# Kernel tuning notes

Measured on AMD Instinct MI355X. Metric: run time of the kernel, lower is better.

Reference implementation:

```python
import jax, jax.numpy as jnp
import numpy as np
from jax.scipy.special import erf

# ---- static config (mirrors module __init__) ----
G = 64          # graphs per batch
N = 64          # atoms per graph (equal-size graphs)
T = G * N       # total atoms
NUM_TYPES = 4
DEG = 32        # avg neighbors per atom
E = T * DEG
F = 128         # node feature dim
R_MAX = 6.0
R_IN = 1.0
EPS = 0.5       # fill value for distance matrix / cross-graph gamma
Q_TOT = 0.0


def setup_inputs() -> dict:
    key = jax.random.key(0)
    ks = jax.random.split(key, 12)
    batch = jnp.repeat(jnp.arange(G, dtype=jnp.int64), N)
    types = jax.random.randint(ks[0], (T,), 0, NUM_TYPES)
    node_attrs = jax.nn.one_hot(types, NUM_TYPES, dtype=jnp.float32)
    # within-graph random edges, symmetrized
    src = jax.random.randint(ks[1], (E // 2,), 0, T)
    dst = (src // N) * N + jax.random.randint(ks[2], (E // 2,), 0, N)
    edge_index = jnp.stack([jnp.concatenate([src, dst]),
                            jnp.concatenate([dst, src])]).astype(jnp.int64)
    half_len = jax.random.uniform(ks[3], (E // 2,), minval=1.0, maxval=R_MAX, dtype=jnp.float32)
    edge_length = jnp.concatenate([half_len, half_len])[:, None]
    kappa = jax.random.normal(ks[4], (T,), dtype=jnp.float32)
    node_feats = jax.random.normal(ks[5], (T, F), dtype=jnp.float32)
    ref_eta = jax.random.uniform(ks[6], (NUM_TYPES,), minval=0.5, maxval=1.5, dtype=jnp.float32)
    ref_log_sigma = jax.random.normal(ks[7], (NUM_TYPES,), dtype=jnp.float32) * 0.1
    ref_A = jax.random.uniform(ks[8], (NUM_TYPES, NUM_TYPES), minval=10.0, maxval=50.0, dtype=jnp.float32)
    ref_B = jax.random.uniform(ks[9], (NUM_TYPES, NUM_TYPES), minval=2.0, maxval=4.0, dtype=jnp.float32)
    ref_C = jax.random.uniform(ks[10], (NUM_TYPES, NUM_TYPES), minval=100.0, maxval=300.0, dtype=jnp.float32)
    ref_D = jnp.zeros((NUM_TYPES, NUM_TYPES), dtype=jnp.float32)
    ref_mu = jax.random.uniform(ks[11], (NUM_TYPES, NUM_TYPES), minval=0.8, maxval=1.2, dtype=jnp.float32)
    # symmetrize pairwise refs (type-pair parameters)
    sym = lambda m: 0.5 * (m + m.T)
    short_energy = jax.random.normal(jax.random.fold_in(key, 100), (G, 1), dtype=jnp.float32)
    atomic_short_energy = jax.random.normal(jax.random.fold_in(key, 101), (T, 1), dtype=jnp.float32)
    return dict(batch=batch, node_attrs=node_attrs, edge_index=edge_index,
                edge_length=edge_length, kappa=kappa, node_feats=node_feats,
                ref_eta=ref_eta, ref_log_sigma=ref_log_sigma,
                ref_A=sym(ref_A), ref_B=sym(ref_B), ref_C=sym(ref_C),
                ref_D=ref_D, ref_mu=sym(ref_mu),
                short_energy=short_energy, atomic_short_energy=atomic_short_energy)


def _f_cut(R):
    c1 = jnp.tanh(1.0) ** 3
    in1 = (R > 0.0) & (R < R_IN)
    in2 = (R >= R_IN) & (R <= R_MAX)
    smooth = jnp.tanh(1.0 - (R - R_IN) / (R_MAX - R_IN)) ** 3
    return jnp.where(in1, c1, jnp.where(in2, smooth, 0.0))


def reference(batch, node_attrs, edge_index, edge_length, kappa, node_feats,
              ref_eta, ref_log_sigma, ref_A, ref_B, ref_C, ref_D, ref_mu,
              short_energy, atomic_short_energy):
    types = jnp.argmax(node_attrs, axis=1)              # [T]
    ref_sigma = jnp.exp(ref_log_sigma)
    sigma = ref_sigma[types]                            # [T]
    eta = ref_eta[types]                                # [T]
    ref_gamma = jnp.sqrt(ref_sigma[:, None] ** 2 + ref_sigma[None, :] ** 2)
    same = batch[:, None] == batch[None, :]             # [T,T] block mask
    tij = (types[:, None], types[None, :])
    gamma = jnp.where(same, ref_gamma[tij], EPS)

    # dense distance matrix: eps fill, edge distances scattered in
    R = jnp.full((T, T), EPS, dtype=jnp.float32)
    R = R.at[edge_index[0], edge_index[1]].set(edge_length[:, 0])
    Fc = _f_cut(R)

    factor = erf(R / (jnp.sqrt(2.0) * gamma)) / R       # [T,T]
    sqrt_pi = jnp.sqrt(jnp.pi).astype(jnp.float32)
    A_ij = jnp.diag(eta + 1.0 / (sigma * sqrt_pi)) + factor
    A_tril = jnp.tril(A_ij)

    # per-graph diagonal blocks -> extended (N+1) charge-equilibration solve
    A4 = A_tril.reshape(G, N, G, N)
    g = jnp.arange(G)
    A_blocks = A4[g, :, g, :]                           # [G,N,N]
    A_ext = jnp.zeros((G, N + 1, N + 1), dtype=jnp.float32)
    A_ext = A_ext.at[:, :N, :N].set(A_blocks)
    A_ext = A_ext.at[:, N, :N].set(1.0).at[:, :N, N].set(1.0)
    kappa_ext = jnp.concatenate([kappa.reshape(G, N),
                                 jnp.full((G, 1), Q_TOT, dtype=jnp.float32)], axis=1)
    sol = jnp.linalg.solve(A_ext, -kappa_ext[..., None])[..., 0]  # [G,N+1]
    charges = sol[:, :N].reshape(T)                     # drop Lagrange multiplier

    atomic_potentials = (factor * Fc) @ charges         # [T]
    E_factor = jnp.diag(0.5 / (sigma * sqrt_pi)) + factor
    V = E_factor @ charges
    atomic_E_el = charges * V                           # [T]
    E_el = jax.ops.segment_sum(atomic_E_el, batch, num_segments=G)[:, None]

    # two-body short-range repulsion/dispersion
    pair = lambda ref: jnp.where(same, ref[tij], 0.0)
    Am, Bm, Cm, Dm, mum = pair(ref_A), pair(ref_B), pair(ref_C), pair(ref_D), pair(ref_mu)
    E2b_ij = (Am * jnp.exp(Bm * (mum - R)) - Cm / R ** 6 - Dm / R ** 8) * Fc
    E2b_ij = E2b_ij * (1.0 - jnp.eye(T, dtype=jnp.float32))
    atomic_E2b = (E2b_ij.sum(axis=-1) * 0.5)[:, None]   # [T,1]
    E_2b = jax.ops.segment_sum(atomic_E2b, batch, num_segments=G)  # [G,1]

    E_tot = E_el + E_2b + short_energy                  # [G,1]
    node_energy = atomic_E_el[:, None] + atomic_E2b + atomic_short_energy
    node_feats_out = jnp.concatenate([node_feats, charges[:, None],
                                      atomic_potentials[:, None]], axis=1)
    return E_tot, node_energy, charges, node_feats_out
```

## Files before the change

### kernel.cpp

```cpp
#include <hip/hip_runtime.h>

#define G 64
#define NN 64
#define TT 4096
#define EDGES 131072

#define OUT_ETOT 0
#define OUT_NODEE 64
#define OUT_Q (64 + 4096)
#define OUT_NF (64 + 4096 + 4096)

__device__ __forceinline__ float wave_sum_f(float v) {
#pragma unroll
    for (int m = 1; m < 64; m <<= 1) v += __shfl_xor(v, m);
    return v;
}
__device__ __forceinline__ double wave_sum_d(double v) {
#pragma unroll
    for (int m = 1; m < 64; m <<= 1) v += __shfl_xor(v, m);
    return v;
}
__device__ __forceinline__ double bcast_d(double v, int j) {
    union { double d; int i[2]; } u;
    u.d = v;
    union { int i[2]; double d; } r;
    r.i[0] = __builtin_amdgcn_readlane(u.i[0], j);
    r.i[1] = __builtin_amdgcn_readlane(u.i[1], j);
    return r.d;
}
__device__ __forceinline__ int type_of(float4 na) {
    int t = 0;
    float best = na.x;
    if (na.y > best) { best = na.y; t = 1; }
    if (na.z > best) { best = na.z; t = 2; }
    if (na.w > best) { best = na.w; t = 3; }
    return t;
}

__global__ void k_scatter(const int* __restrict__ ei, int* __restrict__ winner) {
    int e = blockIdx.x * blockDim.x + threadIdx.x;
    if (e >= EDGES) return;
    int i = ei[e];
    int j = ei[EDGES + e];
    atomicMax(&winner[(i << 6) + (j & 63)], e);
}

__global__ __launch_bounds__(256) void k_build(
    const float* __restrict__ node_attrs, const float* __restrict__ edge_len,
    const int* __restrict__ winner, const float* __restrict__ ref_log_sigma,
    const float* __restrict__ ref_A, const float* __restrict__ ref_B,
    const float* __restrict__ ref_C, const float* __restrict__ ref_D,
    const float* __restrict__ ref_mu,
    float* __restrict__ factor_g, float* __restrict__ fcf_g,
    float* __restrict__ aE2b) {
    const int row = blockIdx.x * 4 + (threadIdx.x >> 6);
    const int lane = threadIdx.x & 63;
    const int g = row >> 6;
    const int ir = row & 63;
    const float th1 = tanhf(1.0f);
    const float c1 = th1 * th1 * th1;

    const int wdx = winner[(row << 6) + lane];
    const float4 na = *(const float4*)(node_attrs + ((size_t)((g << 6) + lane) << 2));

    const float R = (wdx >= 0) ? edge_len[wdx] : 0.5f;
    const int tj = type_of(na);
    const int ti = __shfl(tj, ir);
    const float sgj = __expf(ref_log_sigma[tj]);
    const float sgi = __shfl(sgj, ir);
    const float gam = sqrtf(sgi * sgi + sgj * sgj);

    const float rinv = __frcp_rn(R);
    const float factor = erff(R * (0.70710678118654752f / gam)) * rinv;
    float fc;
    if (R < 1.0f) fc = c1;
    else if (R <= 6.0f) {
        float x = 1.0f - (R - 1.0f) * 0.2f;
        float ex = __expf(2.0f * x);
        float t = (ex - 1.0f) / (ex + 1.0f);
        fc = t * t * t;
    } else fc = 0.0f;

    factor_g[(row << 6) + lane] = factor;
    fcf_g[(row << 6) + lane] = factor * fc;

    float e = 0.0f;
    if (ir != lane) {
        int t4 = ti * 4 + tj;
        float r2 = rinv * rinv;
        float r6 = r2 * r2 * r2;
        e = (ref_A[t4] * __expf(ref_B[t4] * (ref_mu[t4] - R)) - ref_C[t4] * r6 -
             ref_D[t4] * (r6 * r2)) * fc;
    }
    e = wave_sum_f(e);
    if (lane == 0) aE2b[row] = 0.5f * e;
}

__global__ __launch_bounds__(256) void k_solve(
    const float* __restrict__ factor_g, const float* __restrict__ node_attrs,
    const float* __restrict__ kappa, const float* __restrict__ ref_eta,
    const float* __restrict__ ref_log_sigma,
    float* __restrict__ qc, float* __restrict__ qsum) {
    __shared__ float sL[64][65];
    __shared__ float s_diag[64];
    const int g = blockIdx.x;
    const int tid = threadIdx.x;
    const float SQRT_PI = 1.7724538509055159f;

    const float4* src4 = (const float4*)(factor_g + ((size_t)g << 12));
#pragma unroll
    for (int k = 0; k < 4; ++k) {
        int f = k * 256 + tid;
        float4 v = src4[f];
        int rr = f >> 4, cc = (f & 15) << 2;
        sL[rr][cc] = v.x; sL[rr][cc + 1] = v.y;
        sL[rr][cc + 2] = v.z; sL[rr][cc + 3] = v.w;
    }
    if (tid < 64) {
        float4 na = *(const float4*)(node_attrs + ((size_t)((g << 6) + tid) << 2));
        int t = type_of(na);
        float sg = __expf(ref_log_sigma[t]);
        s_diag[tid] = ref_eta[t] + 1.0f / (sg * SQRT_PI);
    }
    __syncthreads();

    if (tid < 64) {
        const int i = tid;
        double Ld = (double)(s_diag[i] + sL[i][i]);
        double inv = 1.0 / Ld;
        double au = 1.0;
        double av = (double)kappa[(g << 6) + i];
        double my_u = 0.0, my_v = 0.0;
        for (int j = 0; j < 64; ++j) {
            double ij = bcast_d(inv, j);
            double uj = bcast_d(au, j) * ij;
            double vj = bcast_d(av, j) * ij;
            if (i == j) { my_u = uj; my_v = vj; }
            if (i > j) {
                double Lij = (double)sL[i][j];
                au -= Lij * uj;
                av -= Lij * vj;
            }
        }
        double Su = wave_sum_d(my_u);
        double Sv = wave_sum_d(my_v);
        double lam = Sv / Su;
        float q = (float)(-my_v + lam * my_u);
        qc[(g << 6) + i] = q;
        float sq = wave_sum_f(q);
        if (i == 0) qsum[g] = sq;
    }
}

__global__ __launch_bounds__(256) void k_final(
    const float* __restrict__ factor_g, const float* __restrict__ fcf_g,
    const float* __restrict__ qc, const float* __restrict__ qsum,
    const float* __restrict__ aE2b, const float* __restrict__ node_attrs,
    const float* __restrict__ ref_log_sigma,
    const float* __restrict__ atomic_short, const float* __restrict__ nf_in,
    float* __restrict__ aEel_ws, float* __restrict__ out) {
    const int i = blockIdx.x * 4 + (threadIdx.x >> 6);
    const int lane = threadIdx.x & 63;
    const int g = i >> 6;
    const float SQRT_PI = 1.7724538509055159f;
    const float th1 = tanhf(1.0f);
    const float c1 = th1 * th1 * th1;
    const float factor_off = erff(0.70710678118654752f / 0.5f) * 2.0f;

    const float qj = qc[(g << 6) + lane];
    const float f = factor_g[(i << 6) + lane];
    const float fcf = fcf_g[(i << 6) + lane];
    const float qs = qsum[lane];
    const float2 v2 = ((const float2*)nf_in)[(i << 6) + lane];
    const float4 na = *(const float4*)(node_attrs + ((size_t)i << 2));

    float p = fcf * qj;
    float w = f * qj;
#pragma unroll
    for (int m = 1; m < 64; m <<= 1) {
        p += __shfl_xor(p, m);
        w += __shfl_xor(w, m);
    }
    float Qall = wave_sum_f(qs);

    *(float2*)(out + OUT_NF + (size_t)i * 130 + lane * 2) = v2;

    if (lane == 0) {
        float off = Qall - qsum[g];
        int t = type_of(na);
        float sg = __expf(ref_log_sigma[t]);
        float coef = 0.5f / (sg * SQRT_PI);
        float q = qc[i];
        float ap = p + factor_off * c1 * off;
        float V = w + factor_off * off + coef * q;
        float aEel = q * V;
        aEel_ws[i] = aEel;
        out[OUT_NODEE + i] = aEel + aE2b[i] + atomic_short[i];
        out[OUT_Q + i] = q;
        out[OUT_NF + (size_t)i * 130 + 128] = q;
        out[OUT_NF + (size_t)i * 130 + 129] = ap;
    }
}

__global__ void k_etot(const float* __restrict__ aEel,
                       const float* __restrict__ aE2b,
                       const float* __restrict__ short_e,
                       float* __restrict__ out) {
    int g = blockIdx.x;
    int lane = threadIdx.x;
    float v = aEel[(g << 6) + lane] + aE2b[(g << 6) + lane];
    v = wave_sum_f(v);
    if (lane == 0) out[OUT_ETOT + g] = v + short_e[g];
}

extern "C" void kernel_launch(void* const* d_in, const int* in_sizes, int n_in,
                              void* d_out, int out_size, void* d_ws, size_t ws_size,
                              hipStream_t stream) {
    const float* node_attrs = (const float*)d_in[1];
    const int* edge_index = (const int*)d_in[2];
    const float* edge_length = (const float*)d_in[3];
    const float* kappa = (const float*)d_in[4];
    const float* node_feats = (const float*)d_in[5];
    const float* ref_eta = (const float*)d_in[6];
    const float* ref_log_sigma = (const float*)d_in[7];
    const float* ref_A = (const float*)d_in[8];
    const float* ref_B = (const float*)d_in[9];
    const float* ref_C = (const float*)d_in[10];
    const float* ref_D = (const float*)d_in[11];
    const float* ref_mu = (const float*)d_in[12];
    const float* short_energy = (const float*)d_in[13];
    const float* atomic_short = (const float*)d_in[14];

    float* out = (float*)d_out;
    char* ws = (char*)d_ws;
    int* winner = (int*)ws;
    float* factor_g = (float*)(ws + (1 << 20));
    float* fcf_g = factor_g + TT * 64;
    float* aE2b = fcf_g + TT * 64;
    float* qc = aE2b + TT;
    float* qsum = qc + TT;
    float* aEel = qsum + G;

    hipMemsetAsync(winner, 0xFF, (size_t)TT * 64 * sizeof(int), stream);
    k_scatter<<<EDGES / 256, 256, 0, stream>>>(edge_index, winner);
    k_build<<<TT / 4, 256, 0, stream>>>(node_attrs, edge_length, winner,
                                        ref_log_sigma, ref_A, ref_B, ref_C,
                                        ref_D, ref_mu, factor_g, fcf_g, aE2b);
    k_solve<<<G, 256, 0, stream>>>(factor_g, node_attrs, kappa, ref_eta,
                                   ref_log_sigma, qc, qsum);
    k_final<<<TT / 4, 256, 0, stream>>>(factor_g, fcf_g, qc, qsum, aE2b,
                                        node_attrs, ref_log_sigma, atomic_short,
                                        node_feats, aEel, out);
    k_etot<<<G, 64, 0, stream>>>(aEel, aE2b, short_energy, out);
}
```

Baseline: 33.82 us.

## Pack edge index and length into 64-bit atomics and fuse build/etot kernels

```diff
diff --git a/kernel.cpp b/kernel.cpp
--- a/kernel.cpp
+++ b/kernel.cpp
@@ -9,6 +9,8 @@
 #define OUT_NODEE 64
 #define OUT_Q (64 + 4096)
 #define OUT_NF (64 + 4096 + 4096)
+
+typedef unsigned long long ull;
 
 __device__ __forceinline__ float wave_sum_f(float v) {
 #pragma unroll
@@ -36,91 +38,58 @@
     if (na.w > best) { best = na.w; t = 3; }
     return t;
 }
-
-__global__ void k_scatter(const int* __restrict__ ei, int* __restrict__ winner) {
+__device__ __forceinline__ float fcut(float R, float c1) {
+    if (R < 1.0f) return c1;
+    if (R > 6.0f) return 0.0f;
+    float x = 1.0f - (R - 1.0f) * 0.2f;
+    float ex = __expf(2.0f * x);
+    float t = (ex - 1.0f) / (ex + 1.0f);
+    return t * t * t;
+}
+
+__global__ __launch_bounds__(256) void k_scatter(const int* __restrict__ ei,
+                                                 const float* __restrict__ elen,
+                                                 ull* __restrict__ packed) {
     int e = blockIdx.x * blockDim.x + threadIdx.x;
     if (e >= EDGES) return;
     int i = ei[e];
     int j = ei[EDGES + e];
-    atomicMax(&winner[(i << 6) + (j & 63)], e);
-}
-
-__global__ __launch_bounds__(256) void k_build(
-    const float* __restrict__ node_attrs, const float* __restrict__ edge_len,
-    const int* __restrict__ winner, const float* __restrict__ ref_log_sigma,
-    const float* __restrict__ ref_A, const float* __restrict__ ref_B,
-    const float* __restrict__ ref_C, const float* __restrict__ ref_D,
-    const float* __restrict__ ref_mu,
-    float* __restrict__ factor_g, float* __restrict__ fcf_g,
-    float* __restrict__ aE2b) {
-    const int row = blockIdx.x * 4 + (threadIdx.x >> 6);
-    const int lane = threadIdx.x & 63;
-    const int g = row >> 6;
-    const int ir = row & 63;
-    const float th1 = tanhf(1.0f);
-    const float c1 = th1 * th1 * th1;
-
-    const int wdx = winner[(row << 6) + lane];
-    const float4 na = *(const float4*)(node_attrs + ((size_t)((g << 6) + lane) << 2));
-
-    const float R = (wdx >= 0) ? edge_len[wdx] : 0.5f;
-    const int tj = type_of(na);
-    const int ti = __shfl(tj, ir);
-    const float sgj = __expf(ref_log_sigma[tj]);
-    const float sgi = __shfl(sgj, ir);
-    const float gam = sqrtf(sgi * sgi + sgj * sgj);
-
-    const float rinv = __frcp_rn(R);
-    const float factor = erff(R * (0.70710678118654752f / gam)) * rinv;
-    float fc;
-    if (R < 1.0f) fc = c1;
-    else if (R <= 6.0f) {
-        float x = 1.0f - (R - 1.0f) * 0.2f;
-        float ex = __expf(2.0f * x);
-        float t = (ex - 1.0f) / (ex + 1.0f);
-        fc = t * t * t;
-    } else fc = 0.0f;
-
-    factor_g[(row << 6) + lane] = factor;
-    fcf_g[(row << 6) + lane] = factor * fc;
-
-    float e = 0.0f;
-    if (ir != lane) {
-        int t4 = ti * 4 + tj;
-        float r2 = rinv * rinv;
-        float r6 = r2 * r2 * r2;
-        e = (ref_A[t4] * __expf(ref_B[t4] * (ref_mu[t4] - R)) - ref_C[t4] * r6 -
-             ref_D[t4] * (r6 * r2)) * fc;
-    }
-    e = wave_sum_f(e);
-    if (lane == 0) aE2b[row] = 0.5f * e;
+    float R = elen[e];
+    ull v = ((ull)(unsigned)e << 32) | (ull)__float_as_uint(R);
+    atomicMax(&packed[(i << 6) + (j & 63)], v);
 }
 
 __global__ __launch_bounds__(256) void k_solve(
-    const float* __restrict__ factor_g, const float* __restrict__ node_attrs,
+    const ull* __restrict__ packed, const float* __restrict__ node_attrs,
     const float* __restrict__ kappa, const float* __restrict__ ref_eta,
-    const float* __restrict__ ref_log_sigma,
-    float* __restrict__ qc, float* __restrict__ qsum) {
+    const float* __restrict__ ref_log_sigma, const float* __restrict__ short_e,
+    float* __restrict__ qc, float* __restrict__ qsum, float* __restrict__ out) {
     __shared__ float sL[64][65];
+    __shared__ float s_sig[64];
     __shared__ float s_diag[64];
     const int g = blockIdx.x;
     const int tid = threadIdx.x;
     const float SQRT_PI = 1.7724538509055159f;
 
-    const float4* src4 = (const float4*)(factor_g + ((size_t)g << 12));
-#pragma unroll
-    for (int k = 0; k < 4; ++k) {
-        int f = k * 256 + tid;
-        float4 v = src4[f];
-        int rr = f >> 4, cc = (f & 15) << 2;
-        sL[rr][cc] = v.x; sL[rr][cc + 1] = v.y;
-        sL[rr][cc + 2] = v.z; sL[rr][cc + 3] = v.w;
-    }
     if (tid < 64) {
         float4 na = *(const float4*)(node_attrs + ((size_t)((g << 6) + tid) << 2));
         int t = type_of(na);
         float sg = __expf(ref_log_sigma[t]);
+        s_sig[tid] = sg;
         s_diag[tid] = ref_eta[t] + 1.0f / (sg * SQRT_PI);
+    }
+    if (tid == 64) out[OUT_ETOT + g] = short_e[g];
+    __syncthreads();
+
+#pragma unroll
+    for (int k = 0; k < 16; ++k) {
+        int c = k * 256 + tid;
+        int row = c >> 6, col = c & 63;
+        ull pk = packed[((size_t)g << 12) + c];
+        float R = (pk > 0ull) ? __uint_as_float((unsigned)pk) : 0.5f;
+        float sr = s_sig[row], sc = s_sig[col];
+        float gam = sqrtf(sr * sr + sc * sc);
+        sL[row][col] = erff(R * (0.70710678118654752f / gam)) * __frcp_rn(R);
     }
     __syncthreads();
 
@@ -153,64 +122,74 @@
 }
 
 __global__ __launch_bounds__(256) void k_final(
-    const float* __restrict__ factor_g, const float* __restrict__ fcf_g,
-    const float* __restrict__ qc, const float* __restrict__ qsum,
-    const float* __restrict__ aE2b, const float* __restrict__ node_attrs,
-    const float* __restrict__ ref_log_sigma,
+    const ull* __restrict__ packed, const float* __restrict__ qc,
+    const float* __restrict__ qsum, const float* __restrict__ node_attrs,
+    const float* __restrict__ ref_log_sigma, const float* __restrict__ ref_A,
+    const float* __restrict__ ref_B, const float* __restrict__ ref_C,
+    const float* __restrict__ ref_D, const float* __restrict__ ref_mu,
     const float* __restrict__ atomic_short, const float* __restrict__ nf_in,
-    float* __restrict__ aEel_ws, float* __restrict__ out) {
+    float* __restrict__ out) {
     const int i = blockIdx.x * 4 + (threadIdx.x >> 6);
     const int lane = threadIdx.x & 63;
     const int g = i >> 6;
+    const int ir = i & 63;
     const float SQRT_PI = 1.7724538509055159f;
     const float th1 = tanhf(1.0f);
     const float c1 = th1 * th1 * th1;
     const float factor_off = erff(0.70710678118654752f / 0.5f) * 2.0f;
 
+    const ull pk = packed[((size_t)i << 6) + lane];
     const float qj = qc[(g << 6) + lane];
-    const float f = factor_g[(i << 6) + lane];
-    const float fcf = fcf_g[(i << 6) + lane];
     const float qs = qsum[lane];
     const float2 v2 = ((const float2*)nf_in)[(i << 6) + lane];
-    const float4 na = *(const float4*)(node_attrs + ((size_t)i << 2));
-
-    float p = fcf * qj;
-    float w = f * qj;
+    const float4 na = *(const float4*)(node_attrs + ((size_t)((g << 6) + lane) << 2));
+
+    const int tj = type_of(na);
+    const int ti = __shfl(tj, ir);
+    const float sgj = __expf(ref_log_sigma[tj]);
+    const float sgi = __shfl(sgj, ir);
+    const float gam = sqrtf(sgi * sgi + sgj * sgj);
+
+    const float R = (pk > 0ull) ? __uint_as_float((unsigned)pk) : 0.5f;
+    const float rinv = __frcp_rn(R);
+    const float factor = erff(R * (0.70710678118654752f / gam)) * rinv;
+    const float fc = fcut(R, c1);
+
+    float e = 0.0f;
+    if (ir != lane) {
+        int t4 = ti * 4 + tj;
+        float r2 = rinv * rinv;
+        float r6 = r2 * r2 * r2;
+        e = (ref_A[t4] * __expf(ref_B[t4] * (ref_mu[t4] - R)) - ref_C[t4] * r6 -
+             ref_D[t4] * (r6 * r2)) * fc;
+    }
+    float p = factor * fc * qj;
+    float w = factor * qj;
 #pragma unroll
     for (int m = 1; m < 64; m <<= 1) {
         p += __shfl_xor(p, m);
         w += __shfl_xor(w, m);
-    }
-    float Qall = wave_sum_f(qs);
+        e += __shfl_xor(e, m);
+    }
+    const float Qall = wave_sum_f(qs);
+    const float qsg = __shfl(qs, g);
+    const float q = __shfl(qj, ir);
 
     *(float2*)(out + OUT_NF + (size_t)i * 130 + lane * 2) = v2;
 
     if (lane == 0) {
-        float off = Qall - qsum[g];
-        int t = type_of(na);
-        float sg = __expf(ref_log_sigma[t]);
-        float coef = 0.5f / (sg * SQRT_PI);
-        float q = qc[i];
+        float off = Qall - qsg;
+        float aE2b = 0.5f * e;
+        float coef = 0.5f / (sgi * SQRT_PI);
         float ap = p + factor_off * c1 * off;
         float V = w + factor_off * off + coef * q;
         float aEel = q * V;
-        aEel_ws[i] = aEel;
-        out[OUT_NODEE + i] = aEel + aE2b[i] + atomic_short[i];
+        out[OUT_NODEE + i] = aEel + aE2b + atomic_short[i];
         out[OUT_Q + i] = q;
         out[OUT_NF + (size_t)i * 130 + 128] = q;
         out[OUT_NF + (size_t)i * 130 + 129] = ap;
-    }
-}
-
-__global__ void k_etot(const float* __restrict__ aEel,
-                       const float* __restrict__ aE2b,
-                       const float* __restrict__ short_e,
-                       float* __restrict__ out) {
-    int g = blockIdx.x;
-    int lane = threadIdx.x;
-    float v = aEel[(g << 6) + lane] + aE2b[(g << 6) + lane];
-    v = wave_sum_f(v);
-    if (lane == 0) out[OUT_ETOT + g] = v + short_e[g];
+        atomicAdd(&out[OUT_ETOT + g], aEel + aE2b);
+    }
 }
 
 extern "C" void kernel_launch(void* const* d_in, const int* in_sizes, int n_in,
@@ -233,23 +212,16 @@
 
     float* out = (float*)d_out;
     char* ws = (char*)d_ws;
-    int* winner = (int*)ws;
-    float* factor_g = (float*)(ws + (1 << 20));
-    float* fcf_g = factor_g + TT * 64;
-    float* aE2b = fcf_g + TT * 64;
-    float* qc = aE2b + TT;
+    ull* packed = (ull*)ws;
+    float* qc = (float*)(ws + (2u << 20));
     float* qsum = qc + TT;
-    float* aEel = qsum + G;
-
-    hipMemsetAsync(winner, 0xFF, (size_t)TT * 64 * sizeof(int), stream);
-    k_scatter<<<EDGES / 256, 256, 0, stream>>>(edge_index, winner);
-    k_build<<<TT / 4, 256, 0, stream>>>(node_attrs, edge_length, winner,
+
+    hipMemsetAsync(packed, 0, (size_t)TT * 64 * sizeof(ull), stream);
+    k_scatter<<<EDGES / 256, 256, 0, stream>>>(edge_index, edge_length, packed);
+    k_solve<<<G, 256, 0, stream>>>(packed, node_attrs, kappa, ref_eta,
+                                   ref_log_sigma, short_energy, qc, qsum, out);
+    k_final<<<TT / 4, 256, 0, stream>>>(packed, qc, qsum, node_attrs,
                                         ref_log_sigma, ref_A, ref_B, ref_C,
-                                        ref_D, ref_mu, factor_g, fcf_g, aE2b);
-    k_solve<<<G, 256, 0, stream>>>(factor_g, node_attrs, kappa, ref_eta,
-                                   ref_log_sigma, qc, qsum);
-    k_final<<<TT / 4, 256, 0, stream>>>(factor_g, fcf_g, qc, qsum, aE2b,
-                                        node_attrs, ref_log_sigma, atomic_short,
-                                        node_feats, aEel, out);
-    k_etot<<<G, 64, 0, stream>>>(aEel, aE2b, short_energy, out);
-}
+                                        ref_D, ref_mu, atomic_short, node_feats,
+                                        out);
+}
```

After: 62.60 us. 1.85x slower.
